# Kernel optimization log

Measured on AMD Instinct MI355X. Metric: run time of the kernel, lower is better.

Reference implementation:

```python
import jax, jax.numpy as jnp
import numpy as np
from jax import lax

RWKV_K_CLAMP = 60.0
RWKV_K_EPS = 1e-8


def setup_inputs() -> dict:
    key = jax.random.key(0)
    ks = jax.random.split(key, 12)
    B, T, C = 4, 1024, 1024
    s = 1.0 / np.sqrt(C)  # scaled linear weights so exp(k) stays sane
    return {
        "xq": jax.random.normal(ks[0], (B, T, C), jnp.float32),
        "xk": jax.random.normal(ks[1], (B, T, C), jnp.float32),
        "xv": jax.random.normal(ks[2], (B, T, C), jnp.float32),
        "time_decay": jax.random.normal(ks[3], (C, 1), jnp.float32) * 0.1,
        "time_first": jnp.full((C, 1), np.log(0.3), jnp.float32),
        "time_mix_k": jax.random.uniform(ks[4], (1, 1, C), jnp.float32),
        "time_mix_v": jax.random.uniform(ks[5], (1, 1, C), jnp.float32),
        "time_mix_r": jax.random.uniform(ks[6], (1, 1, C), jnp.float32),
        "Wk": jax.random.normal(ks[7], (C, C), jnp.float32) * s,
        "Wv": jax.random.normal(ks[8], (C, C), jnp.float32) * s,
        "Wr": jax.random.normal(ks[9], (C, C), jnp.float32) * s,
        "Wo": jax.random.normal(ks[10], (C, C), jnp.float32) * s,
    }


def reference(xq, xk, xv, time_decay, time_first, time_mix_k, time_mix_v,
              time_mix_r, Wk, Wv, Wr, Wo):
    B, T, C = xq.shape
    x = xq  # module only uses xq
    # time_shift: ZeroPad2d((0,0,1,-1)) -> xx[t] = x[t-1], xx[0] = 0
    xx = jnp.pad(x, ((0, 0), (1, 0), (0, 0)))[:, :T]
    k = jnp.einsum('btc,dc->btd', x * time_mix_k + xx * (1 - time_mix_k), Wk)
    v = jnp.einsum('btc,dc->btd', x * time_mix_v + xx * (1 - time_mix_v), Wv)
    r = jnp.einsum('btc,dc->btd', x * time_mix_r + xx * (1 - time_mix_r), Wr)
    sr = jax.nn.sigmoid(r)

    kc = jnp.exp(jnp.minimum(k, RWKV_K_CLAMP)).transpose(0, 2, 1)  # [B,C,T]
    vc = v.transpose(0, 2, 1)                                       # [B,C,T]
    kv = kc * vc

    # time_curve (ctx_len == T): [-(T-2), ..., -1, 0], length T-1
    curve = jnp.arange(T - 1, dtype=jnp.float32) - (T - 2)
    time_w = jnp.concatenate(
        [jnp.exp(time_decay) * curve[None, :], time_first], axis=-1)  # [C,T]
    w = jnp.exp(time_w)[:, None, :]  # conv kernel [C,1,T]

    def dconv(a):  # causal grouped conv1d (torch conv1d == cross-correlation)
        ap = jnp.pad(a, ((0, 0), (0, 0), (T - 1, 0)))
        return lax.conv_general_dilated(
            ap, w, (1,), 'VALID', feature_group_count=C,
            dimension_numbers=('NCH', 'OIH', 'NCH'))

    wkv = dconv(kv)
    wk = dconv(kc) + RWKV_K_EPS
    out = sr * (wkv / wk).transpose(0, 2, 1)  # [B,T,C]
    return jnp.einsum('btc,dc->btd', out, Wo)
```

## Files before the change

kernel.cpp:

```cpp
#include <hip/hip_runtime.h>
#include <math.h>

constexpr int B = 4, T = 1024, C = 1024, D = 1024;
constexpr int M = B * T;
constexpr float K_CLAMP = 60.0f, K_EPS = 1e-8f;

typedef _Float16 half8 __attribute__((ext_vector_type(8)));
typedef _Float16 half4v __attribute__((ext_vector_type(4)));
typedef float float4v __attribute__((ext_vector_type(4)));

typedef __attribute__((address_space(3))) unsigned int lds_uint;
typedef const __attribute__((address_space(1))) unsigned int g_uint;
__device__ __forceinline__ void load_lds16(const void* g, void* l) {
    __builtin_amdgcn_global_load_lds((g_uint*)(size_t)g,
                                     (lds_uint*)(unsigned int)(size_t)l, 16, 0, 0);
}

__global__ __launch_bounds__(256) void prep_kernel(
    const float* __restrict__ x, const float* __restrict__ tmk,
    const float* __restrict__ tmv, const float* __restrict__ tmr,
    _Float16* __restrict__ ak, _Float16* __restrict__ av, _Float16* __restrict__ ar)
{
    const int gid = blockIdx.x * 256 + threadIdx.x;
    const int m = gid >> 8;
    const int cg = (gid & 255) << 2;
    const int t = m & (T - 1);
    float4 xv = *(const float4*)(x + (size_t)m * C + cg);
    float4 xp = make_float4(0.f, 0.f, 0.f, 0.f);
    if (t != 0) xp = *(const float4*)(x + (size_t)(m - 1) * C + cg);
    float4 k4 = *(const float4*)(tmk + cg);
    float4 v4 = *(const float4*)(tmv + cg);
    float4 r4 = *(const float4*)(tmr + cg);
    half4v ok, ov, orr;
    ok[0] = (_Float16)(xv.x * k4.x + xp.x * (1.f - k4.x));
    ok[1] = (_Float16)(xv.y * k4.y + xp.y * (1.f - k4.y));
    ok[2] = (_Float16)(xv.z * k4.z + xp.z * (1.f - k4.z));
    ok[3] = (_Float16)(xv.w * k4.w + xp.w * (1.f - k4.w));
    ov[0] = (_Float16)(xv.x * v4.x + xp.x * (1.f - v4.x));
    ov[1] = (_Float16)(xv.y * v4.y + xp.y * (1.f - v4.y));
    ov[2] = (_Float16)(xv.z * v4.z + xp.z * (1.f - v4.z));
    ov[3] = (_Float16)(xv.w * v4.w + xp.w * (1.f - v4.w));
    orr[0] = (_Float16)(xv.x * r4.x + xp.x * (1.f - r4.x));
    orr[1] = (_Float16)(xv.y * r4.y + xp.y * (1.f - r4.y));
    orr[2] = (_Float16)(xv.z * r4.z + xp.z * (1.f - r4.z));
    orr[3] = (_Float16)(xv.w * r4.w + xp.w * (1.f - r4.w));
    *(half4v*)(ak + (size_t)m * C + cg) = ok;
    *(half4v*)(av + (size_t)m * C + cg) = ov;
    *(half4v*)(ar + (size_t)m * C + cg) = orr;
}

__global__ __launch_bounds__(256) void wcvt_kernel(
    const float* __restrict__ w0, const float* __restrict__ w1,
    const float* __restrict__ w2, const float* __restrict__ w3,
    _Float16* __restrict__ h0, _Float16* __restrict__ h1,
    _Float16* __restrict__ h2, _Float16* __restrict__ h3)
{
    const int mat = blockIdx.y;
    const float* s = mat == 0 ? w0 : mat == 1 ? w1 : mat == 2 ? w2 : w3;
    _Float16* d = mat == 0 ? h0 : mat == 1 ? h1 : mat == 2 ? h2 : h3;
    const int gid = blockIdx.x * 256 + threadIdx.x;
    float4 v = *(const float4*)(s + (size_t)gid * 4);
    half4v o;
    o[0] = (_Float16)v.x; o[1] = (_Float16)v.y;
    o[2] = (_Float16)v.z; o[3] = (_Float16)v.w;
    *(half4v*)(d + (size_t)gid * 4) = o;
}

__device__ __forceinline__ void gemm_core(
    const _Float16* __restrict__ A, const _Float16* __restrict__ W,
    _Float16* lA, _Float16* lB, float4v acc[4][4])
{
    const int tid = threadIdx.x, wave = tid >> 6, lane = tid & 63;
    const int quad = lane >> 4, l15 = lane & 15;
    const int wm = wave & 1, wn = wave >> 1;

    const int s0 = tid, s1 = 256 + tid;
    const int r0 = s0 >> 2, kc0 = ((s0 & 3) - (r0 >> 1)) & 3;
    const int r1 = s1 >> 2, kc1 = ((s1 & 3) - (r1 >> 1)) & 3;
    const _Float16* a0 = A + (size_t)r0 * C + kc0 * 8;
    const _Float16* a1 = A + (size_t)r1 * C + kc1 * 8;
    const _Float16* b0 = W + (size_t)r0 * C + kc0 * 8;
    const _Float16* b1 = W + (size_t)r1 * C + kc1 * 8;
    _Float16* dA0 = lA + (size_t)(wave * 64) * 8;
    _Float16* dA1 = lA + (size_t)(256 + wave * 64) * 8;
    _Float16* dB0 = lB + (size_t)(wave * 64) * 8;
    _Float16* dB1 = lB + (size_t)(256 + wave * 64) * 8;

    int aOff[4], bOff[4];
#pragma unroll
    for (int i = 0; i < 4; i++) {
        int mm = wm * 64 + i * 16 + l15;
        aOff[i] = (mm * 4 + ((quad + (mm >> 1)) & 3)) * 8;
        int nn = wn * 64 + i * 16 + l15;
        bOff[i] = (nn * 4 + ((quad + (nn >> 1)) & 3)) * 8;
    }

    for (int k0 = 0; k0 < C; k0 += 32) {
        load_lds16(a0, dA0);
        load_lds16(a1, dA1);
        load_lds16(b0, dB0);
        load_lds16(b1, dB1);
        a0 += 32; a1 += 32; b0 += 32; b1 += 32;
        __syncthreads();
        half8 af[4], bf[4];
#pragma unroll
        for (int i = 0; i < 4; i++) af[i] = *(const half8*)(lA + aOff[i]);
#pragma unroll
        for (int i = 0; i < 4; i++) bf[i] = *(const half8*)(lB + bOff[i]);
#pragma unroll
        for (int i = 0; i < 4; i++)
#pragma unroll
            for (int j = 0; j < 4; j++)
                acc[i][j] = __builtin_amdgcn_mfma_f32_16x16x32_f16(af[i], bf[j], acc[i][j], 0, 0, 0);
        __syncthreads();
    }
}

__global__ __launch_bounds__(256) void gemm_in_kernel(
    const _Float16* __restrict__ ak, const _Float16* __restrict__ av, const _Float16* __restrict__ ar,
    const _Float16* __restrict__ wk, const _Float16* __restrict__ wv, const _Float16* __restrict__ wr,
    _Float16* __restrict__ kc, _Float16* __restrict__ vv, _Float16* __restrict__ sr)
{
    __shared__ _Float16 lA[128 * 32];
    __shared__ _Float16 lB[128 * 32];
    const int mat = blockIdx.y >> 3;
    const int ntile = (blockIdx.y & 7) * 128;
    const int mtile = blockIdx.x * 128;
    const _Float16* A = (mat == 0 ? ak : mat == 1 ? av : ar) + (size_t)mtile * C;
    const _Float16* W = (mat == 0 ? wk : mat == 1 ? wv : wr) + (size_t)ntile * C;
    _Float16* Y = mat == 0 ? kc : mat == 1 ? vv : sr;

    float4v acc[4][4] = {};
    gemm_core(A, W, lA, lB, acc);

    const int tid = threadIdx.x, wave = tid >> 6, lane = tid & 63;
    const int quad = lane >> 4, l15 = lane & 15;
    const int wm = wave & 1, wn = wave >> 1;
    const int bidx = mtile >> 10;
    const int tbase = (mtile & (T - 1)) + wm * 64;
#pragma unroll
    for (int i = 0; i < 4; i++) {
#pragma unroll
        for (int j = 0; j < 4; j++) {
            const int d = ntile + wn * 64 + j * 16 + l15;
            const int t0 = tbase + i * 16 + quad * 4;
            half4v o;
#pragma unroll
            for (int r = 0; r < 4; r++) {
                float v = acc[i][j][r];
                if (mat == 0) v = expf(fminf(v, K_CLAMP));
                else if (mat == 2) v = 1.0f / (1.0f + expf(-v));
                o[r] = (_Float16)v;
            }
            *(half4v*)(Y + (((size_t)(bidx * D + d)) << 10) + t0) = o;
        }
    }
}

__global__ __launch_bounds__(256) void gemm_out_kernel(
    const _Float16* __restrict__ midT, const _Float16* __restrict__ wo,
    float* __restrict__ out)
{
    __shared__ _Float16 lA[128 * 32];
    __shared__ _Float16 lB[128 * 32];
    const int mtile = blockIdx.x * 128;
    const int ntile = blockIdx.y * 128;
    float4v acc[4][4] = {};
    gemm_core(midT + (size_t)mtile * C, wo + (size_t)ntile * C, lA, lB, acc);

    const int tid = threadIdx.x, wave = tid >> 6, lane = tid & 63;
    const int quad = lane >> 4, l15 = lane & 15;
    const int wm = wave & 1, wn = wave >> 1;
#pragma unroll
    for (int i = 0; i < 4; i++) {
#pragma unroll
        for (int j = 0; j < 4; j++) {
            const int dcol = ntile + wn * 64 + j * 16 + l15;
#pragma unroll
            for (int r = 0; r < 4; r++) {
                const int m = mtile + wm * 64 + i * 16 + quad * 4 + r;
                out[(size_t)m * D + dcol] = acc[i][j][r];
            }
        }
    }
}

__global__ __launch_bounds__(256) void scan_kernel(
    const _Float16* __restrict__ kc, const _Float16* __restrict__ vv,
    const _Float16* __restrict__ sr, const float* __restrict__ td,
    const float* __restrict__ tf, _Float16* __restrict__ mid)
{
    const int gtid = blockIdx.x * 256 + threadIdx.x;
    const int wave = gtid >> 6;
    const int lane = threadIdx.x & 63;
    const int c = wave & (C - 1);
    const int bidx = wave >> 10;
    const float wfac = expf(-expf(td[c]));
    const float ef = expf(tf[c]);
    const size_t base = (((size_t)(bidx * C + c)) << 10) + lane * 16;

    half8 kA = *(const half8*)(kc + base), kB = *(const half8*)(kc + base + 8);
    half8 vA = *(const half8*)(vv + base), vB = *(const half8*)(vv + base + 8);
    half8 sA = *(const half8*)(sr + base), sB = *(const half8*)(sr + base + 8);
    float kcl[16], vl[16], srl[16];
#pragma unroll
    for (int i = 0; i < 8; i++) {
        kcl[i] = (float)kA[i]; kcl[8 + i] = (float)kB[i];
        vl[i]  = (float)vA[i]; vl[8 + i]  = (float)vB[i];
        srl[i] = (float)sA[i]; srl[8 + i] = (float)sB[i];
    }
    float ua = 0.f, ub = 0.f;
#pragma unroll
    for (int i = 0; i < 16; i++) {
        float kv = kcl[i] * vl[i];
        ua = fmaf(wfac, ua, kv);
        ub = fmaf(wfac, ub, kcl[i]);
    }
    float w2 = wfac * wfac, w4 = w2 * w2, w8 = w4 * w4, w16 = w8 * w8;
    float f = w16, sa = ua, sb = ub;
#pragma unroll
    for (int off = 1; off < 64; off <<= 1) {
        float pa = __shfl_up(sa, off);
        float pb = __shfl_up(sb, off);
        if (lane >= off) { sa = fmaf(f, pa, sa); sb = fmaf(f, pb, sb); }
        f = f * f;
    }
    float a0 = __shfl_up(sa, 1);
    float b0 = __shfl_up(sb, 1);
    if (lane == 0) { a0 = 0.f; b0 = 0.f; }
    half8 o0, o1;
#pragma unroll
    for (int i = 0; i < 16; i++) {
        float kv = kcl[i] * vl[i];
        float wkv = fmaf(ef, kv, a0);
        float wk = fmaf(ef, kcl[i], b0) + K_EPS;
        float o = srl[i] * (wkv / wk);
        if (i < 8) o0[i] = (_Float16)o; else o1[i - 8] = (_Float16)o;
        a0 = fmaf(wfac, a0, kv);
        b0 = fmaf(wfac, b0, kcl[i]);
    }
    *(half8*)(mid + base) = o0;
    *(half8*)(mid + base + 8) = o1;
}

__global__ __launch_bounds__(256) void transpose_kernel(
    const _Float16* __restrict__ mid, _Float16* __restrict__ midT)
{
    __shared__ _Float16 tile[64][72];
    const int b = blockIdx.z;
    const int ct = blockIdx.y * 64;
    const int tt = blockIdx.x * 64;
    const int tid = threadIdx.x;
#pragma unroll
    for (int it = 0; it < 2; it++) {
        const int cc = (tid >> 3) + it * 32;
        const int t8 = (tid & 7) * 8;
        half8 v = *(const half8*)(mid + (((size_t)(b * C + ct + cc)) << 10) + tt + t8);
#pragma unroll
        for (int j = 0; j < 8; j++) tile[t8 + j][cc] = v[j];
    }
    __syncthreads();
#pragma unroll
    for (int it = 0; it < 2; it++) {
        const int t = (tid >> 3) + it * 32;
        const int c8 = (tid & 7) * 8;
        half8 v;
#pragma unroll
        for (int j = 0; j < 8; j++) v[j] = tile[t][c8 + j];
        *(half8*)(midT + (((size_t)(b * T + tt + t)) << 10) + ct + c8) = v;
    }
}

extern "C" void kernel_launch(void* const* d_in, const int* in_sizes, int n_in,
                              void* d_out, int out_size, void* d_ws, size_t ws_size,
                              hipStream_t stream) {
    const float* xq  = (const float*)d_in[0];
    const float* td  = (const float*)d_in[3];
    const float* tf  = (const float*)d_in[4];
    const float* tmk = (const float*)d_in[5];
    const float* tmv = (const float*)d_in[6];
    const float* tmr = (const float*)d_in[7];
    const float* Wk  = (const float*)d_in[8];
    const float* Wv  = (const float*)d_in[9];
    const float* Wr  = (const float*)d_in[10];
    const float* Wo  = (const float*)d_in[11];
    float* out = (float*)d_out;

    const size_t MC = (size_t)M * C;
    char* ws = (char*)d_ws;
    _Float16* ak   = (_Float16*)(ws);
    _Float16* av   = (_Float16*)(ws + MC * 2);
    _Float16* ar   = (_Float16*)(ws + MC * 4);
    _Float16* wk16 = (_Float16*)(ws + MC * 6);
    _Float16* wv16 = wk16 + (size_t)D * C;
    _Float16* wr16 = wv16 + (size_t)D * C;
    _Float16* wo16 = wr16 + (size_t)D * C;
    _Float16* kc16 = (_Float16*)(ws + MC * 6 + (size_t)D * C * 8);
    _Float16* vv16 = kc16 + MC;
    _Float16* sr16 = vv16 + MC;
    _Float16* mid  = ak;
    _Float16* midT = av;

    prep_kernel<<<dim3(M * C / 4 / 256), dim3(256), 0, stream>>>(
        xq, tmk, tmv, tmr, ak, av, ar);
    wcvt_kernel<<<dim3(D * C / 4 / 256, 4), dim3(256), 0, stream>>>(
        Wk, Wv, Wr, Wo, wk16, wv16, wr16, wo16);
    gemm_in_kernel<<<dim3(M / 128, 24), dim3(256), 0, stream>>>(
        ak, av, ar, wk16, wv16, wr16, kc16, vv16, sr16);
    scan_kernel<<<dim3(B * C * 64 / 256), dim3(256), 0, stream>>>(
        kc16, vv16, sr16, td, tf, mid);
    transpose_kernel<<<dim3(T / 64, C / 64, B), dim3(256), 0, stream>>>(
        mid, midT);
    gemm_out_kernel<<<dim3(M / 128, D / 128), dim3(256), 0, stream>>>(
        midT, wo16, out);
}
```

Before: 209.2 us.

## Deepen GEMM K-tile to 64, shrink output GEMM M-tile, use fast exp/sigmoid

Both GEMMs now stage a 64-wide K slice per iteration with an 8-way XOR swizzle, which halves the number of barrier pairs per tile and doubles the MFMA work done between syncs. The output GEMM uses 64x128 tiles, doubling its block count so more CUs have work. The input GEMM epilogue switches to __expf and a reciprocal-based sigmoid to make the activation cheaper, at a small cost in accuracy. The deeper tile doubles LDS use per block, which may reduce occupancy.

Result: faster. 188.1 us (-10.1%).

```diff
diff --git a/kernel.cpp b/kernel.cpp
--- a/kernel.cpp
+++ b/kernel.cpp
@@ -14,6 +14,10 @@
 __device__ __forceinline__ void load_lds16(const void* g, void* l) {
     __builtin_amdgcn_global_load_lds((g_uint*)(size_t)g,
                                      (lds_uint*)(unsigned int)(size_t)l, 16, 0, 0);
+}
+
+__device__ __forceinline__ float fast_sigmoid(float v) {
+    return __builtin_amdgcn_rcpf(1.0f + __expf(-v));
 }
 
 __global__ __launch_bounds__(256) void prep_kernel(
@@ -66,78 +70,69 @@
     *(half4v*)(d + (size_t)gid * 4) = o;
 }
 
-__device__ __forceinline__ void gemm_core(
-    const _Float16* __restrict__ A, const _Float16* __restrict__ W,
-    _Float16* lA, _Float16* lB, float4v acc[4][4])
-{
-    const int tid = threadIdx.x, wave = tid >> 6, lane = tid & 63;
-    const int quad = lane >> 4, l15 = lane & 15;
-    const int wm = wave & 1, wn = wave >> 1;
-
-    const int s0 = tid, s1 = 256 + tid;
-    const int r0 = s0 >> 2, kc0 = ((s0 & 3) - (r0 >> 1)) & 3;
-    const int r1 = s1 >> 2, kc1 = ((s1 & 3) - (r1 >> 1)) & 3;
-    const _Float16* a0 = A + (size_t)r0 * C + kc0 * 8;
-    const _Float16* a1 = A + (size_t)r1 * C + kc1 * 8;
-    const _Float16* b0 = W + (size_t)r0 * C + kc0 * 8;
-    const _Float16* b1 = W + (size_t)r1 * C + kc1 * 8;
-    _Float16* dA0 = lA + (size_t)(wave * 64) * 8;
-    _Float16* dA1 = lA + (size_t)(256 + wave * 64) * 8;
-    _Float16* dB0 = lB + (size_t)(wave * 64) * 8;
-    _Float16* dB1 = lB + (size_t)(256 + wave * 64) * 8;
-
-    int aOff[4], bOff[4];
-#pragma unroll
-    for (int i = 0; i < 4; i++) {
-        int mm = wm * 64 + i * 16 + l15;
-        aOff[i] = (mm * 4 + ((quad + (mm >> 1)) & 3)) * 8;
-        int nn = wn * 64 + i * 16 + l15;
-        bOff[i] = (nn * 4 + ((quad + (nn >> 1)) & 3)) * 8;
-    }
-
-    for (int k0 = 0; k0 < C; k0 += 32) {
-        load_lds16(a0, dA0);
-        load_lds16(a1, dA1);
-        load_lds16(b0, dB0);
-        load_lds16(b1, dB1);
-        a0 += 32; a1 += 32; b0 += 32; b1 += 32;
-        __syncthreads();
-        half8 af[4], bf[4];
-#pragma unroll
-        for (int i = 0; i < 4; i++) af[i] = *(const half8*)(lA + aOff[i]);
-#pragma unroll
-        for (int i = 0; i < 4; i++) bf[i] = *(const half8*)(lB + bOff[i]);
-#pragma unroll
-        for (int i = 0; i < 4; i++)
-#pragma unroll
-            for (int j = 0; j < 4; j++)
-                acc[i][j] = __builtin_amdgcn_mfma_f32_16x16x32_f16(af[i], bf[j], acc[i][j], 0, 0, 0);
-        __syncthreads();
-    }
-}
-
 __global__ __launch_bounds__(256) void gemm_in_kernel(
     const _Float16* __restrict__ ak, const _Float16* __restrict__ av, const _Float16* __restrict__ ar,
     const _Float16* __restrict__ wk, const _Float16* __restrict__ wv, const _Float16* __restrict__ wr,
     _Float16* __restrict__ kc, _Float16* __restrict__ vv, _Float16* __restrict__ sr)
 {
-    __shared__ _Float16 lA[128 * 32];
-    __shared__ _Float16 lB[128 * 32];
+    __shared__ _Float16 lA[128 * 64];
+    __shared__ _Float16 lB[128 * 64];
+    const int tid = threadIdx.x, wave = tid >> 6, lane = tid & 63;
+    const int quad = lane >> 4, l15 = lane & 15;
+    const int wm = wave & 1, wn = wave >> 1;
     const int mat = blockIdx.y >> 3;
     const int ntile = (blockIdx.y & 7) * 128;
     const int mtile = blockIdx.x * 128;
     const _Float16* A = (mat == 0 ? ak : mat == 1 ? av : ar) + (size_t)mtile * C;
     const _Float16* W = (mat == 0 ? wk : mat == 1 ? wv : wr) + (size_t)ntile * C;
-    _Float16* Y = mat == 0 ? kc : mat == 1 ? vv : sr;
+
+    const int rS = tid >> 3, oS = tid & 7, cS = (oS - rS) & 7;
+    const _Float16* pA = A + (size_t)rS * C + cS * 8;
+    const _Float16* pB = W + (size_t)rS * C + cS * 8;
+
+    int aOff[4], bOff[4];
+#pragma unroll
+    for (int i = 0; i < 4; i++) {
+        int mm = wm * 64 + i * 16 + l15;
+        aOff[i] = mm * 64 + (((quad + mm) & 7) << 3);
+        int nn = wn * 64 + i * 16 + l15;
+        bOff[i] = nn * 64 + (((quad + nn) & 7) << 3);
+    }
 
     float4v acc[4][4] = {};
-    gemm_core(A, W, lA, lB, acc);
-
-    const int tid = threadIdx.x, wave = tid >> 6, lane = tid & 63;
-    const int quad = lane >> 4, l15 = lane & 15;
-    const int wm = wave & 1, wn = wave >> 1;
+    for (int it = 0; it < 16; it++) {
+#pragma unroll
+        for (int n = 0; n < 4; n++) {
+            load_lds16(pA + (size_t)n * 32 * C, lA + (n * 256 + wave * 64) * 8);
+            load_lds16(pB + (size_t)n * 32 * C, lB + (n * 256 + wave * 64) * 8);
+        }
+        pA += 64; pB += 64;
+        __syncthreads();
+        half8 af[4], bf[4];
+#pragma unroll
+        for (int i = 0; i < 4; i++) af[i] = *(const half8*)(lA + aOff[i]);
+#pragma unroll
+        for (int j = 0; j < 4; j++) bf[j] = *(const half8*)(lB + bOff[j]);
+#pragma unroll
+        for (int i = 0; i < 4; i++)
+#pragma unroll
+            for (int j = 0; j < 4; j++)
+                acc[i][j] = __builtin_amdgcn_mfma_f32_16x16x32_f16(af[i], bf[j], acc[i][j], 0, 0, 0);
+#pragma unroll
+        for (int i = 0; i < 4; i++) af[i] = *(const half8*)(lA + (aOff[i] ^ 32));
+#pragma unroll
+        for (int j = 0; j < 4; j++) bf[j] = *(const half8*)(lB + (bOff[j] ^ 32));
+#pragma unroll
+        for (int i = 0; i < 4; i++)
+#pragma unroll
+            for (int j = 0; j < 4; j++)
+                acc[i][j] = __builtin_amdgcn_mfma_f32_16x16x32_f16(af[i], bf[j], acc[i][j], 0, 0, 0);
+        __syncthreads();
+    }
+
     const int bidx = mtile >> 10;
     const int tbase = (mtile & (T - 1)) + wm * 64;
+    _Float16* Y = mat == 0 ? kc : mat == 1 ? vv : sr;
 #pragma unroll
     for (int i = 0; i < 4; i++) {
 #pragma unroll
@@ -148,8 +143,8 @@
 #pragma unroll
             for (int r = 0; r < 4; r++) {
                 float v = acc[i][j][r];
-                if (mat == 0) v = expf(fminf(v, K_CLAMP));
-                else if (mat == 2) v = 1.0f / (1.0f + expf(-v));
+                if (mat == 0) v = __expf(fminf(v, K_CLAMP));
+                else if (mat == 2) v = fast_sigmoid(v);
                 o[r] = (_Float16)v;
             }
             *(half4v*)(Y + (((size_t)(bidx * D + d)) << 10) + t0) = o;
@@ -161,24 +156,71 @@
     const _Float16* __restrict__ midT, const _Float16* __restrict__ wo,
     float* __restrict__ out)
 {
-    __shared__ _Float16 lA[128 * 32];
-    __shared__ _Float16 lB[128 * 32];
-    const int mtile = blockIdx.x * 128;
-    const int ntile = blockIdx.y * 128;
-    float4v acc[4][4] = {};
-    gemm_core(midT + (size_t)mtile * C, wo + (size_t)ntile * C, lA, lB, acc);
-
+    __shared__ _Float16 lA[64 * 64];
+    __shared__ _Float16 lB[128 * 64];
     const int tid = threadIdx.x, wave = tid >> 6, lane = tid & 63;
     const int quad = lane >> 4, l15 = lane & 15;
     const int wm = wave & 1, wn = wave >> 1;
-#pragma unroll
-    for (int i = 0; i < 4; i++) {
+    const int mtile = blockIdx.x * 64;
+    const int ntile = blockIdx.y * 128;
+    const _Float16* A = midT + (size_t)mtile * C;
+    const _Float16* W = wo + (size_t)ntile * C;
+
+    const int rS = tid >> 3, oS = tid & 7, cS = (oS - rS) & 7;
+    const _Float16* pA = A + (size_t)rS * C + cS * 8;
+    const _Float16* pB = W + (size_t)rS * C + cS * 8;
+
+    int aOff[2], bOff[4];
+#pragma unroll
+    for (int i = 0; i < 2; i++) {
+        int mm = wm * 32 + i * 16 + l15;
+        aOff[i] = mm * 64 + (((quad + mm) & 7) << 3);
+    }
+#pragma unroll
+    for (int j = 0; j < 4; j++) {
+        int nn = wn * 64 + j * 16 + l15;
+        bOff[j] = nn * 64 + (((quad + nn) & 7) << 3);
+    }
+
+    float4v acc[2][4] = {};
+    for (int it = 0; it < 16; it++) {
+#pragma unroll
+        for (int n = 0; n < 2; n++)
+            load_lds16(pA + (size_t)n * 32 * C, lA + (n * 256 + wave * 64) * 8);
+#pragma unroll
+        for (int n = 0; n < 4; n++)
+            load_lds16(pB + (size_t)n * 32 * C, lB + (n * 256 + wave * 64) * 8);
+        pA += 64; pB += 64;
+        __syncthreads();
+        half8 af[2], bf[4];
+#pragma unroll
+        for (int i = 0; i < 2; i++) af[i] = *(const half8*)(lA + aOff[i]);
+#pragma unroll
+        for (int j = 0; j < 4; j++) bf[j] = *(const half8*)(lB + bOff[j]);
+#pragma unroll
+        for (int i = 0; i < 2; i++)
+#pragma unroll
+            for (int j = 0; j < 4; j++)
+                acc[i][j] = __builtin_amdgcn_mfma_f32_16x16x32_f16(af[i], bf[j], acc[i][j], 0, 0, 0);
+#pragma unroll
+        for (int i = 0; i < 2; i++) af[i] = *(const half8*)(lA + (aOff[i] ^ 32));
+#pragma unroll
+        for (int j = 0; j < 4; j++) bf[j] = *(const half8*)(lB + (bOff[j] ^ 32));
+#pragma unroll
+        for (int i = 0; i < 2; i++)
+#pragma unroll
+            for (int j = 0; j < 4; j++)
+                acc[i][j] = __builtin_amdgcn_mfma_f32_16x16x32_f16(af[i], bf[j], acc[i][j], 0, 0, 0);
+        __syncthreads();
+    }
+#pragma unroll
+    for (int i = 0; i < 2; i++) {
 #pragma unroll
         for (int j = 0; j < 4; j++) {
             const int dcol = ntile + wn * 64 + j * 16 + l15;
 #pragma unroll
             for (int r = 0; r < 4; r++) {
-                const int m = mtile + wm * 64 + i * 16 + quad * 4 + r;
+                const int m = mtile + wm * 32 + i * 16 + quad * 4 + r;
                 out[(size_t)m * D + dcol] = acc[i][j][r];
             }
         }
@@ -311,6 +353,6 @@
         kc16, vv16, sr16, td, tf, mid);
     transpose_kernel<<<dim3(T / 64, C / 64, B), dim3(256), 0, stream>>>(
         mid, midT);
-    gemm_out_kernel<<<dim3(M / 128, D / 128), dim3(256), 0, stream>>>(
+    gemm_out_kernel<<<dim3(M / 64, D / 128), dim3(256), 0, stream>>>(
         midT, wo16, out);
 }
```
